# Optimization experiments

Measured on AMD Instinct MI355X. Metric: run time of the kernel, lower is better.

Reference implementation:

```python
import jax, jax.numpy as jnp
import numpy as np

B, N, M = 4, 512, 8192
QUERY_DIM, INPUT_DIM = 512, 256
HEADS, DIM_HEAD = 8, 64
ATT_DIM = HEADS * DIM_HEAD  # 512


def setup_inputs() -> dict:
    key = jax.random.key(0)
    ks = jax.random.split(key, 6)
    x = jax.random.normal(ks[0], (B, N, QUERY_DIM), dtype=jnp.float32)
    context = jax.random.normal(ks[1], (B, M, INPUT_DIM), dtype=jnp.float32)
    # Linear weights stored as [in, out] for x @ W
    Wq = jax.random.normal(ks[2], (QUERY_DIM, ATT_DIM), dtype=jnp.float32) / np.sqrt(QUERY_DIM)
    Wkv = jax.random.normal(ks[3], (INPUT_DIM, 2 * ATT_DIM), dtype=jnp.float32) / np.sqrt(INPUT_DIM)
    Wo = jax.random.normal(ks[4], (ATT_DIM, QUERY_DIM), dtype=jnp.float32) / np.sqrt(ATT_DIM)
    bo = jax.random.normal(ks[5], (QUERY_DIM,), dtype=jnp.float32) * 0.01
    return {"x": x, "context": context, "Wq": Wq, "Wkv": Wkv, "Wo": Wo, "bo": bo}


def reference(x, context, Wq, Wkv, Wo, bo):
    scale = DIM_HEAD ** -0.5
    q = x @ Wq                      # [B, N, H*D]
    kv = context @ Wkv              # [B, M, 2*H*D]
    k, v = jnp.split(kv, 2, axis=-1)
    # split heads: b n (h d) -> b h n d
    q = q.reshape(B, N, HEADS, DIM_HEAD).transpose(0, 2, 1, 3)
    k = k.reshape(B, M, HEADS, DIM_HEAD).transpose(0, 2, 1, 3)
    v = v.reshape(B, M, HEADS, DIM_HEAD).transpose(0, 2, 1, 3)
    scores = jnp.einsum('bhid,bhjd->bhij', q, k) * scale  # [B, H, N, M]
    attn = jax.nn.softmax(scores, axis=-1)
    out = jnp.einsum('bhij,bhjd->bhid', attn, v)           # [B, H, N, D]
    out = out.transpose(0, 2, 1, 3).reshape(B, N, ATT_DIM)
    return out @ Wo + bo
```

## Files before the change

### kernel.cpp

```cpp
#include <hip/hip_runtime.h>
#include <hip/hip_bf16.h>
#include <cstdint>

#define NB 4
#define NQ 512
#define NM 8192
#define NH 8
#define DH 64

typedef short bf16x8s __attribute__((ext_vector_type(8)));
typedef float f32x4  __attribute__((ext_vector_type(4)));

static __device__ __forceinline__ short f2bs(float f) {
    unsigned u = __builtin_bit_cast(unsigned, f);
    return (short)(unsigned short)((u + 0x8000u) >> 16);
}
static __device__ __forceinline__ unsigned pk2(float a, float b) {
    unsigned au = __builtin_bit_cast(unsigned, a) + 0x8000u;
    unsigned bu = __builtin_bit_cast(unsigned, b) + 0x8000u;
    return __builtin_amdgcn_perm(bu, au, 0x07060302u);
}

#if __has_builtin(__builtin_amdgcn_exp2f)
static __device__ __forceinline__ float fexp2(float x) { return __builtin_amdgcn_exp2f(x); }
#else
static __device__ __forceinline__ float fexp2(float x) { return exp2f(x); }
#endif

__global__ __launch_bounds__(256) void prep_weights(
    const float* __restrict__ Wq, const float* __restrict__ Wo,
    const float* __restrict__ Wkv,
    short* __restrict__ Wqf, short* __restrict__ Wof, short* __restrict__ Wkvf)
{
    const int t = threadIdx.x;
    const int w = t >> 6, ln = t & 63;
    const int m16 = ln & 15, quad = ln >> 4;
    int f = blockIdx.x * 4 + w;
    const float* src; short* dst; int N, KS, n0, ks;
    if (f < 512)       { src = Wq;  dst = Wqf;  N = 512;  KS = 16; n0 = f >> 4; ks = f & 15; }
    else if (f < 1024) { f -= 512;  src = Wo;  dst = Wof;  N = 512;  KS = 16; n0 = f >> 4; ks = f & 15; }
    else               { f -= 1024; src = Wkv; dst = Wkvf; N = 1024; KS = 8;  n0 = f >> 3; ks = f & 7; }
    const float* sp = src + (size_t)(ks * 32 + quad * 8) * N + n0 * 16 + m16;
    float v[8];
    #pragma unroll
    for (int j = 0; j < 8; ++j) v[j] = sp[(size_t)j * N];
    uint4 pkv = { pk2(v[0],v[1]), pk2(v[2],v[3]), pk2(v[4],v[5]), pk2(v[6],v[7]) };
    *(uint4*)(dst + ((size_t)(n0 * KS + ks) * 64 + ln) * 8) = pkv;
}

__device__ __forceinline__ void proj32_body(
    const float* __restrict__ A, const short* __restrict__ Wf,
    float* __restrict__ C, const float* __restrict__ bias,
    int tm, int tn, char* smemraw)
{
    short* As = (short*)smemraw;

    const int t = threadIdx.x;
    const int w = t >> 6, ln = t & 63;
    const int m16 = ln & 15, quad = ln >> 4;
    const int wm = w >> 1, wn = w & 1;

    const int ar = t >> 3, ac = (t & 7) << 3;

    const float* Ap = A + (size_t)(tm * 32 + ar) * 512 + ac;

    f32x4 acc[2] = {};

    for (int k0 = 0; k0 < 512; k0 += 64) {
        float4 a0 = *(const float4*)(Ap + k0);
        float4 a1 = *(const float4*)(Ap + k0 + 4);
        bf16x8s bfr[2][2];
        #pragma unroll
        for (int ks = 0; ks < 2; ++ks)
            #pragma unroll
            for (int nt = 0; nt < 2; ++nt)
                bfr[ks][nt] = *(const bf16x8s*)(Wf +
                    ((size_t)((tn * 4 + wn * 2 + nt) * 16 + (k0 >> 5) + ks) * 64 + ln) * 8);

        __syncthreads();
        {
            uint4 wa = { pk2(a0.x,a0.y), pk2(a0.z,a0.w), pk2(a1.x,a1.y), pk2(a1.z,a1.w) };
            *(uint4*)&As[ar * 72 + ac] = wa;
        }
        __syncthreads();

        #pragma unroll
        for (int ks = 0; ks < 2; ++ks) {
            bf16x8s af = *(const bf16x8s*)&As[(wm * 16 + m16) * 72 + ks * 32 + quad * 8];
            #pragma unroll
            for (int nt = 0; nt < 2; ++nt)
                acc[nt] = __builtin_amdgcn_mfma_f32_16x16x32_bf16(af, bfr[ks][nt], acc[nt], 0, 0, 0);
        }
    }

    const int row0 = tm * 32 + wm * 16 + quad * 4;
    const int col0 = tn * 64 + wn * 32;
    #pragma unroll
    for (int nt = 0; nt < 2; ++nt) {
        const int col = col0 + nt * 16 + m16;
        const float bb = bias ? bias[col] : 0.f;
        #pragma unroll
        for (int r = 0; r < 4; ++r)
            C[(size_t)(row0 + r) * 512 + col] = acc[nt][r] + bb;
    }
}

__device__ __forceinline__ void kv_body(
    const float* __restrict__ A, const short* __restrict__ Wkvf,
    short* __restrict__ Kf, short* __restrict__ Vf,
    int bid, char* smemraw)
{
    short* As = (short*)smemraw;

    const int t  = threadIdx.x;
    const int tm = bid & 255, tn = bid >> 8;
    const int w  = t >> 6, ln = t & 63;
    const int m16 = ln & 15, quad = ln >> 4;
    const int wm = w & 1, wn = w >> 1;

    const int ar = t >> 3;
    const int ac = (t & 7) << 2;

    const float* Abase = A + (size_t)(tm * 128 + ar) * 256 + ac;

    f32x4 acc[4][4] = {};

    for (int k0 = 0; k0 < 256; k0 += 32) {
        float4 av[4];
        #pragma unroll
        for (int p = 0; p < 4; ++p)
            av[p] = *(const float4*)(Abase + (size_t)p * 32 * 256 + k0);
        bf16x8s bfr[4];
        #pragma unroll
        for (int j = 0; j < 4; ++j)
            bfr[j] = *(const bf16x8s*)(Wkvf +
                ((size_t)((tn * 8 + wn * 4 + j) * 8 + (k0 >> 5)) * 64 + ln) * 8);

        __syncthreads();
        #pragma unroll
        for (int p = 0; p < 4; ++p) {
            uint2 wv = { pk2(av[p].x, av[p].y), pk2(av[p].z, av[p].w) };
            *(uint2*)&As[(p * 32 + ar) * 40 + ac] = wv;
        }
        __syncthreads();

        bf16x8s af[4];
        #pragma unroll
        for (int i = 0; i < 4; ++i)
            af[i] = *(const bf16x8s*)&As[(wm * 64 + i * 16 + m16) * 40 + quad * 8];
        #pragma unroll
        for (int i = 0; i < 4; ++i)
            #pragma unroll
            for (int j = 0; j < 4; ++j)
                acc[i][j] = __builtin_amdgcn_mfma_f32_16x16x32_bf16(af[i], bfr[j], acc[i][j], 0, 0, 0);
    }

    const int col0 = tn * 128 + wn * 64;
    const int row0 = tm * 128 + wm * 64;
    const int b    = row0 >> 13;
    const int mr0  = row0 & (NM - 1);

    if (col0 < 512) {
        const int h = col0 >> 6;
        short* Kp = Kf + (size_t)(b * NH + h) * (NM * DH);
        #pragma unroll
        for (int i = 0; i < 4; ++i)
            #pragma unroll
            for (int j = 0; j < 4; ++j) {
                const int d = j * 16 + m16;
                #pragma unroll
                for (int r = 0; r < 4; ++r) {
                    const int key = mr0 + i * 16 + quad * 4 + r;
                    const int idx = ((key >> 4) * 2 + (d >> 5)) * 512
                                  + (((d >> 3) & 3) * 16 + (key & 15)) * 8 + (d & 7);
                    Kp[idx] = f2bs(acc[i][j][r]);
                }
            }
    } else {
        const int h = (col0 - 512) >> 6;
        short* Vp = Vf + (size_t)(b * NH + h) * (NM * DH);
        #pragma unroll
        for (int i = 0; i < 4; ++i)
            #pragma unroll
            for (int j = 0; j < 4; ++j) {
                const int key0 = mr0 + i * 16 + quad * 4;
                const int idx = (j * 256 + (key0 >> 5)) * 512
                              + ((((key0 >> 3) & 3) * 16 + m16) * 8) + (key0 & 7);
                uint2 pk;
                pk.x = pk2(acc[i][j][0], acc[i][j][1]);
                pk.y = pk2(acc[i][j][2], acc[i][j][3]);
                *(uint2*)(Vp + idx) = pk;
            }
    }
}

__global__ __launch_bounds__(256) void gemm_kvq(
    const float* __restrict__ x,   const short* __restrict__ Wqf, float* __restrict__ q,
    const float* __restrict__ ctx, const short* __restrict__ Wkvf,
    short* __restrict__ Kf, short* __restrict__ Vf)
{
    __shared__ __align__(16) char smem[10240];
    if (blockIdx.x < 512)
        proj32_body(x, Wqf, q, nullptr, (int)(blockIdx.x >> 3), (int)(blockIdx.x & 7), smem);
    else
        kv_body(ctx, Wkvf, Kf, Vf, (int)(blockIdx.x - 512), smem);
}

__global__ __launch_bounds__(256) void gemm_proj32(
    const float* __restrict__ A, const short* __restrict__ Wf,
    float* __restrict__ C, const float* __restrict__ bias)
{
    __shared__ __align__(16) char smem[32 * 72 * 2];
    proj32_body(A, Wf, C, bias, (int)(blockIdx.x >> 3), (int)(blockIdx.x & 7), smem);
}

__global__ __launch_bounds__(256) void attn_mfma(
    const float* __restrict__ Q,
    const short* __restrict__ Kfr,
    const short* __restrict__ Vfr,
    float* __restrict__ Og)
{
    __shared__ __align__(16) float Obuf[4 * 32 * 68];
    __shared__ float lbuf[4 * 32];

    const int bid = blockIdx.x;
    const int xcd = bid & 7, grp = bid >> 3;
    const int bh  = xcd * 4 + (grp & 3);
    const int qt  = grp >> 2;
    const int b   = bh >> 3, h = bh & 7;
    const int t   = threadIdx.x;
    const int w   = t >> 6, ln = t & 63;
    const int m16 = ln & 15, quad = ln >> 4;

    const short* Kbase = Kfr + (size_t)bh * (NM * DH);
    const short* Vbase = Vfr + (size_t)bh * (NM * DH);

    const float qsc = 0.125f * 1.44269504f;
    bf16x8s qf[2][2];
    #pragma unroll
    for (int mt = 0; mt < 2; ++mt) {
        const float* qrow = Q + ((size_t)(b * NQ + qt * 32 + mt * 16 + m16)) * 512 + h * 64;
        #pragma unroll
        for (int ks = 0; ks < 2; ++ks) {
            float4 x0 = *(const float4*)(qrow + ks * 32 + quad * 8);
            float4 x1 = *(const float4*)(qrow + ks * 32 + quad * 8 + 4);
            uint4 pkv = { pk2(x0.x * qsc, x0.y * qsc), pk2(x0.z * qsc, x0.w * qsc),
                          pk2(x1.x * qsc, x1.y * qsc), pk2(x1.z * qsc, x1.w * qsc) };
            qf[mt][ks] = *reinterpret_cast<bf16x8s*>(&pkv);
        }
    }

    bf16x8s ones;
    #pragma unroll
    for (int j = 0; j < 8; ++j) ones[j] = (short)0x3F80;

    f32x4 o[2][4] = {};
    f32x4 lsum[2] = {};

    const int srcLo = (((quad << 1) & 3) << 4) + m16;
    const int srcHi = ((((quad << 1) + 1) & 3) << 4) + m16;
    const bool ktHi = quad >= 2;

    bf16x8s kf[4][2];
    {
        const int kc = w * 64;
        #pragma unroll
        for (int nt = 0; nt < 4; ++nt)
            #pragma unroll
            for (int ks = 0; ks < 2; ++ks)
                kf[nt][ks] = *(const bf16x8s*)(Kbase + ((((kc >> 4) + nt) * 2 + ks) << 9) + ln * 8);
    }

    for (int it = 0; it < 32; ++it) {
        const int kc = it * 256 + w * 64;

        bf16x8s vf[4][2];
        #pragma unroll
        for (int dt = 0; dt < 4; ++dt)
            #pragma unroll
            for (int ks = 0; ks < 2; ++ks)
                vf[dt][ks] = *(const bf16x8s*)(Vbase + ((dt * 256 + (kc >> 5) + ks) << 9) + ln * 8);

        f32x4 st[2][4] = {};
        #pragma unroll
        for (int kt = 0; kt < 4; ++kt)
            #pragma unroll
            for (int mt = 0; mt < 2; ++mt) {
                st[mt][kt] = __builtin_amdgcn_mfma_f32_16x16x32_bf16(kf[kt][0], qf[mt][0], st[mt][kt], 0, 0, 0);
                st[mt][kt] = __builtin_amdgcn_mfma_f32_16x16x32_bf16(kf[kt][1], qf[mt][1], st[mt][kt], 0, 0, 0);
            }

        if (it + 1 < 32) {
            const int kn = (it + 1) * 256 + w * 64;
            #pragma unroll
            for (int nt = 0; nt < 4; ++nt)
                #pragma unroll
                for (int ks = 0; ks < 2; ++ks)
                    kf[nt][ks] = *(const bf16x8s*)(Kbase + ((((kn >> 4) + nt) * 2 + ks) << 9) + ln * 8);
        }

        unsigned pp[2][4][2];
        #pragma unroll
        for (int mt = 0; mt < 2; ++mt)
            #pragma unroll
            for (int kt = 0; kt < 4; ++kt) {
                const float p0 = fexp2(st[mt][kt][0]);
                const float p1 = fexp2(st[mt][kt][1]);
                const float p2 = fexp2(st[mt][kt][2]);
                const float p3 = fexp2(st[mt][kt][3]);
                pp[mt][kt][0] = pk2(p0, p1);
                pp[mt][kt][1] = pk2(p2, p3);
            }

        #pragma unroll
        for (int mt = 0; mt < 2; ++mt)
            #pragma unroll
            for (int ks = 0; ks < 2; ++ks) {
                const unsigned a0 = __shfl(pp[mt][2 * ks][0], srcLo);
                const unsigned b0 = __shfl(pp[mt][2 * ks + 1][0], srcLo);
                const unsigned a1 = __shfl(pp[mt][2 * ks][1], srcLo);
                const unsigned b1 = __shfl(pp[mt][2 * ks + 1][1], srcLo);
                const unsigned a2 = __shfl(pp[mt][2 * ks][0], srcHi);
                const unsigned b2 = __shfl(pp[mt][2 * ks + 1][0], srcHi);
                const unsigned a3 = __shfl(pp[mt][2 * ks][1], srcHi);
                const unsigned b3 = __shfl(pp[mt][2 * ks + 1][1], srcHi);
                uint4 pb;
                pb.x = ktHi ? b0 : a0;
                pb.y = ktHi ? b1 : a1;
                pb.z = ktHi ? b2 : a2;
                pb.w = ktHi ? b3 : a3;
                bf16x8s pbv = *reinterpret_cast<bf16x8s*>(&pb);
                #pragma unroll
                for (int dt = 0; dt < 4; ++dt)
                    o[mt][dt] = __builtin_amdgcn_mfma_f32_16x16x32_bf16(vf[dt][ks], pbv, o[mt][dt], 0, 0, 0);
                lsum[mt] = __builtin_amdgcn_mfma_f32_16x16x32_bf16(ones, pbv, lsum[mt], 0, 0, 0);
            }
    }

    #pragma unroll
    for (int mt = 0; mt < 2; ++mt)
        #pragma unroll
        for (int dt = 0; dt < 4; ++dt)
            *(f32x4*)&Obuf[(w * 32 + mt * 16 + m16) * 68 + dt * 16 + quad * 4] = o[mt][dt];
    if (quad == 0) {
        lbuf[w * 32 +      m16] = lsum[0][0];
        lbuf[w * 32 + 16 + m16] = lsum[1][0];
    }
    __syncthreads();
    {
        const int row = t >> 3, d0 = (t & 7) << 3;
        const float l = lbuf[row] + lbuf[32 + row] + lbuf[64 + row] + lbuf[96 + row];
        const float inv = 1.0f / l;
        float res[8];
        #pragma unroll
        for (int j = 0; j < 8; ++j) {
            float a = Obuf[(row) * 68 + d0 + j]
                    + Obuf[(32 + row) * 68 + d0 + j]
                    + Obuf[(64 + row) * 68 + d0 + j]
                    + Obuf[(96 + row) * 68 + d0 + j];
            res[j] = a * inv;
        }
        float* op = Og + ((size_t)(b * NQ + qt * 32 + row)) * 512 + h * 64 + d0;
        float4 r0 = {res[0], res[1], res[2], res[3]};
        float4 r1 = {res[4], res[5], res[6], res[7]};
        *(float4*)op = r0;
        *(float4*)(op + 4) = r1;
    }
}

extern "C" void kernel_launch(void* const* d_in, const int* in_sizes, int n_in,
                              void* d_out, int out_size, void* d_ws, size_t ws_size,
                              hipStream_t stream) {
    (void)in_sizes; (void)n_in; (void)out_size; (void)ws_size;

    const float* x   = (const float*)d_in[0];
    const float* ctx = (const float*)d_in[1];
    const float* Wq  = (const float*)d_in[2];
    const float* Wkv = (const float*)d_in[3];
    const float* Wo  = (const float*)d_in[4];
    const float* bo  = (const float*)d_in[5];
    float* out = (float*)d_out;

    float* ws    = (float*)d_ws;
    float* q     = ws;
    float* attno = q + (size_t)2048 * 512;
    short* Kf    = (short*)(attno + (size_t)2048 * 512);
    short* Vf    = Kf + (size_t)NB * NH * NM * DH;
    short* Wqf   = Vf + (size_t)NB * NH * NM * DH;
    short* Wof   = Wqf + (size_t)512 * 512;
    short* Wkvf  = Wof + (size_t)512 * 512;

    prep_weights<<<dim3(384), dim3(256), 0, stream>>>(Wq, Wo, Wkv, Wqf, Wof, Wkvf);

    gemm_kvq<<<dim3(2560), dim3(256), 0, stream>>>(x, Wqf, q, ctx, Wkvf, Kf, Vf);

    attn_mfma<<<dim3(512), dim3(256), 0, stream>>>(q, Kf, Vf, attno);

    gemm_proj32<<<dim3(512), dim3(256), 0, stream>>>(attno, Wof, out, bo);
}
```

Before: 191.9 us.

## Split attention keys across blocks and fuse partial reduction into output GEMM

The attention kernel now gives each wave its own 32 query rows (128 per block) and splits the key range into four chunks across blocks, instead of splitting keys across waves and reducing through shared memory. Partial outputs go to a 4x workspace, and row sums are accumulated with atomics into a zeroed buffer. The output-projection GEMM sums the four partials, normalizes by the row sum and applies Wo plus bias. The Q and KV projection GEMMs also drop shared-memory staging and barriers, loading A fragments directly from global memory. This removes in-block syncs and LDS round trips but adds extra global traffic for partials, a memset, and float atomics.

```diff
diff --git a/kernel.cpp b/kernel.cpp
--- a/kernel.cpp
+++ b/kernel.cpp
@@ -48,48 +48,33 @@
     *(uint4*)(dst + ((size_t)(n0 * KS + ks) * 64 + ln) * 8) = pkv;
 }
 
-__device__ __forceinline__ void proj32_body(
+__device__ __forceinline__ void proj_q_body(
     const float* __restrict__ A, const short* __restrict__ Wf,
-    float* __restrict__ C, const float* __restrict__ bias,
-    int tm, int tn, char* smemraw)
-{
-    short* As = (short*)smemraw;
-
+    float* __restrict__ C, int tm, int tn)
+{
     const int t = threadIdx.x;
     const int w = t >> 6, ln = t & 63;
     const int m16 = ln & 15, quad = ln >> 4;
     const int wm = w >> 1, wn = w & 1;
 
-    const int ar = t >> 3, ac = (t & 7) << 3;
-
-    const float* Ap = A + (size_t)(tm * 32 + ar) * 512 + ac;
+    const int row = tm * 32 + wm * 16 + m16;
+    const float* Ap = A + (size_t)row * 512 + quad * 8;
 
     f32x4 acc[2] = {};
 
     for (int k0 = 0; k0 < 512; k0 += 64) {
-        float4 a0 = *(const float4*)(Ap + k0);
-        float4 a1 = *(const float4*)(Ap + k0 + 4);
-        bf16x8s bfr[2][2];
-        #pragma unroll
-        for (int ks = 0; ks < 2; ++ks)
-            #pragma unroll
-            for (int nt = 0; nt < 2; ++nt)
-                bfr[ks][nt] = *(const bf16x8s*)(Wf +
+        #pragma unroll
+        for (int ks = 0; ks < 2; ++ks) {
+            float4 a0 = *(const float4*)(Ap + k0 + ks * 32);
+            float4 a1 = *(const float4*)(Ap + k0 + ks * 32 + 4);
+            uint4 wa = { pk2(a0.x,a0.y), pk2(a0.z,a0.w), pk2(a1.x,a1.y), pk2(a1.z,a1.w) };
+            bf16x8s af = *reinterpret_cast<bf16x8s*>(&wa);
+            #pragma unroll
+            for (int nt = 0; nt < 2; ++nt) {
+                bf16x8s bf = *(const bf16x8s*)(Wf +
                     ((size_t)((tn * 4 + wn * 2 + nt) * 16 + (k0 >> 5) + ks) * 64 + ln) * 8);
-
-        __syncthreads();
-        {
-            uint4 wa = { pk2(a0.x,a0.y), pk2(a0.z,a0.w), pk2(a1.x,a1.y), pk2(a1.z,a1.w) };
-            *(uint4*)&As[ar * 72 + ac] = wa;
-        }
-        __syncthreads();
-
-        #pragma unroll
-        for (int ks = 0; ks < 2; ++ks) {
-            bf16x8s af = *(const bf16x8s*)&As[(wm * 16 + m16) * 72 + ks * 32 + quad * 8];
-            #pragma unroll
-            for (int nt = 0; nt < 2; ++nt)
-                acc[nt] = __builtin_amdgcn_mfma_f32_16x16x32_bf16(af, bfr[ks][nt], acc[nt], 0, 0, 0);
+                acc[nt] = __builtin_amdgcn_mfma_f32_16x16x32_bf16(af, bf, acc[nt], 0, 0, 0);
+            }
         }
     }
 
@@ -98,76 +83,59 @@
     #pragma unroll
     for (int nt = 0; nt < 2; ++nt) {
         const int col = col0 + nt * 16 + m16;
-        const float bb = bias ? bias[col] : 0.f;
         #pragma unroll
         for (int r = 0; r < 4; ++r)
-            C[(size_t)(row0 + r) * 512 + col] = acc[nt][r] + bb;
+            C[(size_t)(row0 + r) * 512 + col] = acc[nt][r];
     }
 }
 
 __device__ __forceinline__ void kv_body(
     const float* __restrict__ A, const short* __restrict__ Wkvf,
-    short* __restrict__ Kf, short* __restrict__ Vf,
-    int bid, char* smemraw)
-{
-    short* As = (short*)smemraw;
-
+    short* __restrict__ Kf, short* __restrict__ Vf, int bid)
+{
     const int t  = threadIdx.x;
     const int tm = bid & 255, tn = bid >> 8;
     const int w  = t >> 6, ln = t & 63;
     const int m16 = ln & 15, quad = ln >> 4;
-    const int wm = w & 1, wn = w >> 1;
-
-    const int ar = t >> 3;
-    const int ac = (t & 7) << 2;
-
-    const float* Abase = A + (size_t)(tm * 128 + ar) * 256 + ac;
-
-    f32x4 acc[4][4] = {};
+
+    const float* Ap0 = A + (size_t)(tm * 128 + w * 32 + m16) * 256 + quad * 8;
+    const float* Ap1 = Ap0 + 16 * 256;
+
+    f32x4 acc[2][8] = {};
 
     for (int k0 = 0; k0 < 256; k0 += 32) {
-        float4 av[4];
-        #pragma unroll
-        for (int p = 0; p < 4; ++p)
-            av[p] = *(const float4*)(Abase + (size_t)p * 32 * 256 + k0);
-        bf16x8s bfr[4];
-        #pragma unroll
-        for (int j = 0; j < 4; ++j)
-            bfr[j] = *(const bf16x8s*)(Wkvf +
-                ((size_t)((tn * 8 + wn * 4 + j) * 8 + (k0 >> 5)) * 64 + ln) * 8);
-
-        __syncthreads();
-        #pragma unroll
-        for (int p = 0; p < 4; ++p) {
-            uint2 wv = { pk2(av[p].x, av[p].y), pk2(av[p].z, av[p].w) };
-            *(uint2*)&As[(p * 32 + ar) * 40 + ac] = wv;
-        }
-        __syncthreads();
-
-        bf16x8s af[4];
-        #pragma unroll
-        for (int i = 0; i < 4; ++i)
-            af[i] = *(const bf16x8s*)&As[(wm * 64 + i * 16 + m16) * 40 + quad * 8];
-        #pragma unroll
-        for (int i = 0; i < 4; ++i)
-            #pragma unroll
-            for (int j = 0; j < 4; ++j)
-                acc[i][j] = __builtin_amdgcn_mfma_f32_16x16x32_bf16(af[i], bfr[j], acc[i][j], 0, 0, 0);
-    }
-
-    const int col0 = tn * 128 + wn * 64;
-    const int row0 = tm * 128 + wm * 64;
+        bf16x8s af[2];
+        {
+            float4 a0 = *(const float4*)(Ap0 + k0);
+            float4 a1 = *(const float4*)(Ap0 + k0 + 4);
+            uint4 wa = { pk2(a0.x,a0.y), pk2(a0.z,a0.w), pk2(a1.x,a1.y), pk2(a1.z,a1.w) };
+            af[0] = *reinterpret_cast<bf16x8s*>(&wa);
+            float4 b0 = *(const float4*)(Ap1 + k0);
+            float4 b1 = *(const float4*)(Ap1 + k0 + 4);
+            uint4 wb = { pk2(b0.x,b0.y), pk2(b0.z,b0.w), pk2(b1.x,b1.y), pk2(b1.z,b1.w) };
+            af[1] = *reinterpret_cast<bf16x8s*>(&wb);
+        }
+        #pragma unroll
+        for (int j = 0; j < 8; ++j) {
+            bf16x8s bfr = *(const bf16x8s*)(Wkvf +
+                ((size_t)((tn * 8 + j) * 8 + (k0 >> 5)) * 64 + ln) * 8);
+            acc[0][j] = __builtin_amdgcn_mfma_f32_16x16x32_bf16(af[0], bfr, acc[0][j], 0, 0, 0);
+            acc[1][j] = __builtin_amdgcn_mfma_f32_16x16x32_bf16(af[1], bfr, acc[1][j], 0, 0, 0);
+        }
+    }
+
+    const int row0 = tm * 128 + w * 32;
     const int b    = row0 >> 13;
     const int mr0  = row0 & (NM - 1);
 
-    if (col0 < 512) {
-        const int h = col0 >> 6;
-        short* Kp = Kf + (size_t)(b * NH + h) * (NM * DH);
-        #pragma unroll
-        for (int i = 0; i < 4; ++i)
-            #pragma unroll
-            for (int j = 0; j < 4; ++j) {
-                const int d = j * 16 + m16;
+    if (tn < 4) {
+        #pragma unroll
+        for (int j = 0; j < 8; ++j) {
+            const int h = tn * 2 + (j >> 2);
+            const int d = (j & 3) * 16 + m16;
+            short* Kp = Kf + (size_t)(b * NH + h) * (NM * DH);
+            #pragma unroll
+            for (int i = 0; i < 2; ++i)
                 #pragma unroll
                 for (int r = 0; r < 4; ++r) {
                     const int key = mr0 + i * 16 + quad * 4 + r;
@@ -175,22 +143,24 @@
                                   + (((d >> 3) & 3) * 16 + (key & 15)) * 8 + (d & 7);
                     Kp[idx] = f2bs(acc[i][j][r]);
                 }
-            }
+        }
     } else {
-        const int h = (col0 - 512) >> 6;
-        short* Vp = Vf + (size_t)(b * NH + h) * (NM * DH);
-        #pragma unroll
-        for (int i = 0; i < 4; ++i)
-            #pragma unroll
-            for (int j = 0; j < 4; ++j) {
+        #pragma unroll
+        for (int j = 0; j < 8; ++j) {
+            const int h = (tn - 4) * 2 + (j >> 2);
+            const int jj = j & 3;
+            short* Vp = Vf + (size_t)(b * NH + h) * (NM * DH);
+            #pragma unroll
+            for (int i = 0; i < 2; ++i) {
                 const int key0 = mr0 + i * 16 + quad * 4;
-                const int idx = (j * 256 + (key0 >> 5)) * 512
+                const int idx = (jj * 256 + (key0 >> 5)) * 512
                               + ((((key0 >> 3) & 3) * 16 + m16) * 8) + (key0 & 7);
                 uint2 pk;
                 pk.x = pk2(acc[i][j][0], acc[i][j][1]);
                 pk.y = pk2(acc[i][j][2], acc[i][j][3]);
                 *(uint2*)(Vp + idx) = pk;
             }
+        }
     }
 }
 
@@ -199,34 +169,24 @@
     const float* __restrict__ ctx, const short* __restrict__ Wkvf,
     short* __restrict__ Kf, short* __restrict__ Vf)
 {
-    __shared__ __align__(16) char smem[10240];
     if (blockIdx.x < 512)
-        proj32_body(x, Wqf, q, nullptr, (int)(blockIdx.x >> 3), (int)(blockIdx.x & 7), smem);
+        proj_q_body(x, Wqf, q, (int)(blockIdx.x >> 3), (int)(blockIdx.x & 7));
     else
-        kv_body(ctx, Wkvf, Kf, Vf, (int)(blockIdx.x - 512), smem);
-}
-
-__global__ __launch_bounds__(256) void gemm_proj32(
-    const float* __restrict__ A, const short* __restrict__ Wf,
-    float* __restrict__ C, const float* __restrict__ bias)
-{
-    __shared__ __align__(16) char smem[32 * 72 * 2];
-    proj32_body(A, Wf, C, bias, (int)(blockIdx.x >> 3), (int)(blockIdx.x & 7), smem);
+        kv_body(ctx, Wkvf, Kf, Vf, (int)(blockIdx.x - 512));
 }
 
 __global__ __launch_bounds__(256) void attn_mfma(
     const float* __restrict__ Q,
     const short* __restrict__ Kfr,
     const short* __restrict__ Vfr,
-    float* __restrict__ Og)
-{
-    __shared__ __align__(16) float Obuf[4 * 32 * 68];
-    __shared__ float lbuf[4 * 32];
-
+    float* __restrict__ Po,
+    float* __restrict__ Lg)
+{
     const int bid = blockIdx.x;
-    const int xcd = bid & 7, grp = bid >> 3;
-    const int bh  = xcd * 4 + (grp & 3);
-    const int qt  = grp >> 2;
+    const int xcd = bid & 7, g = bid >> 3;
+    const int bh  = xcd * 4 + (g & 3);
+    const int qt  = (g >> 2) & 3;
+    const int kq  = g >> 4;
     const int b   = bh >> 3, h = bh & 7;
     const int t   = threadIdx.x;
     const int w   = t >> 6, ln = t & 63;
@@ -239,7 +199,7 @@
     bf16x8s qf[2][2];
     #pragma unroll
     for (int mt = 0; mt < 2; ++mt) {
-        const float* qrow = Q + ((size_t)(b * NQ + qt * 32 + mt * 16 + m16)) * 512 + h * 64;
+        const float* qrow = Q + ((size_t)(b * NQ + qt * 128 + w * 32 + mt * 16 + m16)) * 512 + h * 64;
         #pragma unroll
         for (int ks = 0; ks < 2; ++ks) {
             float4 x0 = *(const float4*)(qrow + ks * 32 + quad * 8);
@@ -263,7 +223,7 @@
 
     bf16x8s kf[4][2];
     {
-        const int kc = w * 64;
+        const int kc = kq * 2048;
         #pragma unroll
         for (int nt = 0; nt < 4; ++nt)
             #pragma unroll
@@ -272,7 +232,7 @@
     }
 
     for (int it = 0; it < 32; ++it) {
-        const int kc = it * 256 + w * 64;
+        const int kc = kq * 2048 + it * 64;
 
         bf16x8s vf[4][2];
         #pragma unroll
@@ -291,7 +251,7 @@
             }
 
         if (it + 1 < 32) {
-            const int kn = (it + 1) * 256 + w * 64;
+            const int kn = kq * 2048 + (it + 1) * 64;
             #pragma unroll
             for (int nt = 0; nt < 4; ++nt)
                 #pragma unroll
@@ -337,34 +297,81 @@
             }
     }
 
-    #pragma unroll
-    for (int mt = 0; mt < 2; ++mt)
+    float* Pq = Po + (size_t)kq * (2048 * 512);
+    #pragma unroll
+    for (int mt = 0; mt < 2; ++mt) {
+        const int row = b * NQ + qt * 128 + w * 32 + mt * 16 + m16;
         #pragma unroll
         for (int dt = 0; dt < 4; ++dt)
-            *(f32x4*)&Obuf[(w * 32 + mt * 16 + m16) * 68 + dt * 16 + quad * 4] = o[mt][dt];
+            *(f32x4*)(Pq + (size_t)row * 512 + h * 64 + dt * 16 + quad * 4) = o[mt][dt];
+    }
     if (quad == 0) {
-        lbuf[w * 32 +      m16] = lsum[0][0];
-        lbuf[w * 32 + 16 + m16] = lsum[1][0];
-    }
-    __syncthreads();
-    {
-        const int row = t >> 3, d0 = (t & 7) << 3;
-        const float l = lbuf[row] + lbuf[32 + row] + lbuf[64 + row] + lbuf[96 + row];
-        const float inv = 1.0f / l;
-        float res[8];
-        #pragma unroll
-        for (int j = 0; j < 8; ++j) {
-            float a = Obuf[(row) * 68 + d0 + j]
-                    + Obuf[(32 + row) * 68 + d0 + j]
-                    + Obuf[(64 + row) * 68 + d0 + j]
-                    + Obuf[(96 + row) * 68 + d0 + j];
-            res[j] = a * inv;
-        }
-        float* op = Og + ((size_t)(b * NQ + qt * 32 + row)) * 512 + h * 64 + d0;
-        float4 r0 = {res[0], res[1], res[2], res[3]};
-        float4 r1 = {res[4], res[5], res[6], res[7]};
-        *(float4*)op = r0;
-        *(float4*)(op + 4) = r1;
+        const int n0 = qt * 128 + w * 32 + m16;
+        atomicAdd(&Lg[(size_t)bh * NQ + n0],      lsum[0][0]);
+        atomicAdd(&Lg[(size_t)bh * NQ + n0 + 16], lsum[1][0]);
+    }
+}
+
+__global__ __launch_bounds__(256) void gemm_out(
+    const float* __restrict__ Po,
+    const float* __restrict__ Lg,
+    const short* __restrict__ Wf,
+    float* __restrict__ C, const float* __restrict__ bias)
+{
+    const int tm = (int)(blockIdx.x >> 3);
+    const int tn = (int)(blockIdx.x & 7);
+    const int t = threadIdx.x;
+    const int w = t >> 6, ln = t & 63;
+    const int m16 = ln & 15, quad = ln >> 4;
+    const int wm = w >> 1, wn = w & 1;
+
+    const int row = tm * 32 + wm * 16 + m16;
+    const int b   = row >> 9, n = row & 511;
+
+    float linv[8];
+    #pragma unroll
+    for (int hh = 0; hh < 8; ++hh)
+        linv[hh] = 1.0f / Lg[(size_t)(b * NH + hh) * NQ + n];
+
+    const float* Ap = Po + (size_t)row * 512 + quad * 8;
+
+    f32x4 acc[2] = {};
+
+    for (int k0 = 0; k0 < 512; k0 += 64) {
+        const float sc = linv[k0 >> 6];
+        #pragma unroll
+        for (int ks = 0; ks < 2; ++ks) {
+            const float* p0 = Ap + k0 + ks * 32;
+            float4 a0 = *(const float4*)(p0);
+            float4 a1 = *(const float4*)(p0 + 4);
+            #pragma unroll
+            for (int qq = 1; qq < 4; ++qq) {
+                float4 c0 = *(const float4*)(p0 + (size_t)qq * (2048 * 512));
+                float4 c1 = *(const float4*)(p0 + (size_t)qq * (2048 * 512) + 4);
+                a0.x += c0.x; a0.y += c0.y; a0.z += c0.z; a0.w += c0.w;
+                a1.x += c1.x; a1.y += c1.y; a1.z += c1.z; a1.w += c1.w;
+            }
+            uint4 wa = { pk2(a0.x * sc, a0.y * sc), pk2(a0.z * sc, a0.w * sc),
+                         pk2(a1.x * sc, a1.y * sc), pk2(a1.z * sc, a1.w * sc) };
+            bf16x8s af = *reinterpret_cast<bf16x8s*>(&wa);
+            #pragma unroll
+            for (int nt = 0; nt < 2; ++nt) {
+                bf16x8s bf = *(const bf16x8s*)(Wf +
+                    ((size_t)((tn * 4 + wn * 2 + nt) * 16 + (k0 >> 5) + ks) * 64 + ln) * 8);
+                acc[nt] = __builtin_amdgcn_mfma_f32_16x16x32_bf16(af, bf, acc[nt], 0, 0, 0);
+            }
+        }
+    }
+
+    const int row0 = tm * 32 + wm * 16 + quad * 4;
+    const int col0 = tn * 64 + wn * 32;
+    #pragma unroll
+    for (int nt = 0; nt < 2; ++nt) {
+        const int col = col0 + nt * 16 + m16;
+        const float bb = bias[col];
+        #pragma unroll
+        for (int r = 0; r < 4; ++r)
+            C[(size_t)(row0 + r) * 512 + col] = acc[nt][r] + bb;
     }
 }
 
@@ -381,20 +388,23 @@
     const float* bo  = (const float*)d_in[5];
     float* out = (float*)d_out;
 
-    float* ws    = (float*)d_ws;
-    float* q     = ws;
-    float* attno = q + (size_t)2048 * 512;
-    short* Kf    = (short*)(attno + (size_t)2048 * 512);
-    short* Vf    = Kf + (size_t)NB * NH * NM * DH;
-    short* Wqf   = Vf + (size_t)NB * NH * NM * DH;
-    short* Wof   = Wqf + (size_t)512 * 512;
-    short* Wkvf  = Wof + (size_t)512 * 512;
+    float* ws   = (float*)d_ws;
+    float* q    = ws;
+    float* Po   = q  + (size_t)2048 * 512;
+    float* Lg   = Po + (size_t)4 * 2048 * 512;
+    short* Kf   = (short*)(Lg + (size_t)32 * 512);
+    short* Vf   = Kf + (size_t)NB * NH * NM * DH;
+    short* Wqf  = Vf + (size_t)NB * NH * NM * DH;
+    short* Wof  = Wqf + (size_t)512 * 512;
+    short* Wkvf = Wof + (size_t)512 * 512;
+
+    hipMemsetAsync(Lg, 0, (size_t)32 * 512 * sizeof(float), stream);
 
     prep_weights<<<dim3(384), dim3(256), 0, stream>>>(Wq, Wo, Wkv, Wqf, Wof, Wkvf);
 
     gemm_kvq<<<dim3(2560), dim3(256), 0, stream>>>(x, Wqf, q, ctx, Wkvf, Kf, Vf);
 
-    attn_mfma<<<dim3(512), dim3(256), 0, stream>>>(q, Kf, Vf, attno);
-
-    gemm_proj32<<<dim3(512), dim3(256), 0, stream>>>(attno, Wof, out, bo);
-}
+    attn_mfma<<<dim3(512), dim3(256), 0, stream>>>(q, Kf, Vf, Po, Lg);
+
+    gemm_out<<<dim3(512), dim3(256), 0, stream>>>(Po, Lg, Wof, out, bo);
+}
```

After: 261.6 us. 36.3% more time.

## Double attention query tile to 64 rows per block to halve K/V reloads

Applied to the files above, without the earlier changes.

Each attention block now handles 64 query rows instead of 32, so every loaded K/V fragment feeds twice as many MFMAs and the grid drops from 512 to 256 blocks. Launch bounds set a minimum of one block per SM, letting the compiler use more registers for the larger accumulators. The cross-wave output reduction now uses two shared buffers with a two-phase add to fit the larger tile in LDS. The trade-off is lower occupancy, fewer blocks than the GPU's 256 CUs can overlap with other work, and higher register pressure.

```diff
diff --git a/kernel.cpp b/kernel.cpp
--- a/kernel.cpp
+++ b/kernel.cpp
@@ -214,19 +214,19 @@
     proj32_body(A, Wf, C, bias, (int)(blockIdx.x >> 3), (int)(blockIdx.x & 7), smem);
 }
 
-__global__ __launch_bounds__(256) void attn_mfma(
+__global__ __launch_bounds__(256, 1) void attn_mfma(
     const float* __restrict__ Q,
     const short* __restrict__ Kfr,
     const short* __restrict__ Vfr,
     float* __restrict__ Og)
 {
-    __shared__ __align__(16) float Obuf[4 * 32 * 68];
-    __shared__ float lbuf[4 * 32];
+    __shared__ __align__(16) float Ob[2][64 * 66];
+    __shared__ float lbuf[4 * 64];
 
     const int bid = blockIdx.x;
-    const int xcd = bid & 7, grp = bid >> 3;
-    const int bh  = xcd * 4 + (grp & 3);
-    const int qt  = grp >> 2;
+    const int xcd = bid & 7, g = bid >> 3;
+    const int bh  = xcd * 4 + (g & 3);
+    const int qt  = g >> 2;
     const int b   = bh >> 3, h = bh & 7;
     const int t   = threadIdx.x;
     const int w   = t >> 6, ln = t & 63;
@@ -236,10 +236,10 @@
     const short* Vbase = Vfr + (size_t)bh * (NM * DH);
 
     const float qsc = 0.125f * 1.44269504f;
-    bf16x8s qf[2][2];
+    bf16x8s qf[4][2];
     #pragma unroll
-    for (int mt = 0; mt < 2; ++mt) {
-        const float* qrow = Q + ((size_t)(b * NQ + qt * 32 + mt * 16 + m16)) * 512 + h * 64;
+    for (int mt = 0; mt < 4; ++mt) {
+        const float* qrow = Q + ((size_t)(b * NQ + qt * 64 + mt * 16 + m16)) * 512 + h * 64;
         #pragma unroll
         for (int ks = 0; ks < 2; ++ks) {
             float4 x0 = *(const float4*)(qrow + ks * 32 + quad * 8);
@@ -254,8 +254,8 @@
     #pragma unroll
     for (int j = 0; j < 8; ++j) ones[j] = (short)0x3F80;
 
-    f32x4 o[2][4] = {};
-    f32x4 lsum[2] = {};
+    f32x4 o[4][4] = {};
+    f32x4 lsum[4] = {};
 
     const int srcLo = (((quad << 1) & 3) << 4) + m16;
     const int srcHi = ((((quad << 1) + 1) & 3) << 4) + m16;
@@ -281,11 +281,11 @@
             for (int ks = 0; ks < 2; ++ks)
                 vf[dt][ks] = *(const bf16x8s*)(Vbase + ((dt * 256 + (kc >> 5) + ks) << 9) + ln * 8);
 
-        f32x4 st[2][4] = {};
+        f32x4 st[4][4] = {};
         #pragma unroll
         for (int kt = 0; kt < 4; ++kt)
             #pragma unroll
-            for (int mt = 0; mt < 2; ++mt) {
+            for (int mt = 0; mt < 4; ++mt) {
                 st[mt][kt] = __builtin_amdgcn_mfma_f32_16x16x32_bf16(kf[kt][0], qf[mt][0], st[mt][kt], 0, 0, 0);
                 st[mt][kt] = __builtin_amdgcn_mfma_f32_16x16x32_bf16(kf[kt][1], qf[mt][1], st[mt][kt], 0, 0, 0);
             }
@@ -299,9 +299,9 @@
                     kf[nt][ks] = *(const bf16x8s*)(Kbase + ((((kn >> 4) + nt) * 2 + ks) << 9) + ln * 8);
         }
 
-        unsigned pp[2][4][2];
-        #pragma unroll
-        for (int mt = 0; mt < 2; ++mt)
+        unsigned pp[4][4][2];
+        #pragma unroll
+        for (int mt = 0; mt < 4; ++mt)
             #pragma unroll
             for (int kt = 0; kt < 4; ++kt) {
                 const float p0 = fexp2(st[mt][kt][0]);
@@ -313,7 +313,7 @@
             }
 
         #pragma unroll
-        for (int mt = 0; mt < 2; ++mt)
+        for (int mt = 0; mt < 4; ++mt)
             #pragma unroll
             for (int ks = 0; ks < 2; ++ks) {
                 const unsigned a0 = __shfl(pp[mt][2 * ks][0], srcLo);
@@ -337,34 +337,49 @@
             }
     }
 
-    #pragma unroll
-    for (int mt = 0; mt < 2; ++mt)
-        #pragma unroll
-        for (int dt = 0; dt < 4; ++dt)
-            *(f32x4*)&Obuf[(w * 32 + mt * 16 + m16) * 68 + dt * 16 + quad * 4] = o[mt][dt];
     if (quad == 0) {
-        lbuf[w * 32 +      m16] = lsum[0][0];
-        lbuf[w * 32 + 16 + m16] = lsum[1][0];
+        #pragma unroll
+        for (int mt = 0; mt < 4; ++mt)
+            lbuf[w * 64 + mt * 16 + m16] = lsum[mt][0];
+    }
+    if ((w & 1) == 0) {
+        float* dst = Ob[w >> 1];
+        #pragma unroll
+        for (int mt = 0; mt < 4; ++mt)
+            #pragma unroll
+            for (int dt = 0; dt < 4; ++dt)
+                *(f32x4*)&dst[(mt * 16 + m16) * 66 + dt * 16 + quad * 4] = o[mt][dt];
+    }
+    __syncthreads();
+    if ((w & 1) == 1) {
+        float* dst = Ob[w >> 1];
+        #pragma unroll
+        for (int mt = 0; mt < 4; ++mt)
+            #pragma unroll
+            for (int dt = 0; dt < 4; ++dt) {
+                float* p = &dst[(mt * 16 + m16) * 66 + dt * 16 + quad * 4];
+                f32x4 cur = *(f32x4*)p;
+                cur += o[mt][dt];
+                *(f32x4*)p = cur;
+            }
     }
     __syncthreads();
     {
-        const int row = t >> 3, d0 = (t & 7) << 3;
-        const float l = lbuf[row] + lbuf[32 + row] + lbuf[64 + row] + lbuf[96 + row];
+        const int row = t >> 2;
+        const int d0  = (t & 3) << 4;
+        const float l = lbuf[row] + lbuf[64 + row] + lbuf[128 + row] + lbuf[192 + row];
         const float inv = 1.0f / l;
-        float res[8];
-        #pragma unroll
-        for (int j = 0; j < 8; ++j) {
-            float a = Obuf[(row) * 68 + d0 + j]
-                    + Obuf[(32 + row) * 68 + d0 + j]
-                    + Obuf[(64 + row) * 68 + d0 + j]
-                    + Obuf[(96 + row) * 68 + d0 + j];
-            res[j] = a * inv;
-        }
-        float* op = Og + ((size_t)(b * NQ + qt * 32 + row)) * 512 + h * 64 + d0;
-        float4 r0 = {res[0], res[1], res[2], res[3]};
-        float4 r1 = {res[4], res[5], res[6], res[7]};
-        *(float4*)op = r0;
-        *(float4*)(op + 4) = r1;
+        float* op = Og + ((size_t)(b * NQ + qt * 64 + row)) * 512 + h * 64 + d0;
+        #pragma unroll
+        for (int j = 0; j < 4; ++j) {
+            const int c = row * 66 + d0 + j * 4;
+            float4 r;
+            r.x = (Ob[0][c + 0] + Ob[1][c + 0]) * inv;
+            r.y = (Ob[0][c + 1] + Ob[1][c + 1]) * inv;
+            r.z = (Ob[0][c + 2] + Ob[1][c + 2]) * inv;
+            r.w = (Ob[0][c + 3] + Ob[1][c + 3]) * inv;
+            *(float4*)(op + j * 4) = r;
+        }
     }
 }
 
@@ -394,7 +409,7 @@
 
     gemm_kvq<<<dim3(2560), dim3(256), 0, stream>>>(x, Wqf, q, ctx, Wkvf, Kf, Vf);
 
-    attn_mfma<<<dim3(512), dim3(256), 0, stream>>>(q, Kf, Vf, attno);
+    attn_mfma<<<dim3(256), dim3(256), 0, stream>>>(q, Kf, Vf, attno);
 
     gemm_proj32<<<dim3(512), dim3(256), 0, stream>>>(attno, Wof, out, bo);
 }
```

Result: slower. 207.8 us (+8.3%).
